# Performance work log

Hardware: AMD Instinct MI355X
Metric: run time of the kernel (lower is better)

The kernel has to match this reference:

```python
import jax, jax.numpy as jnp
import numpy as np

N, D_IN, D_H, D_ATT, C_CLUST, N_CLS = 10000, 1024, 512, 256, 10, 4


def setup_inputs() -> dict:
    key = jax.random.key(0)
    ks = jax.random.split(key, 20)
    s = 0.02
    return {
        "x": jax.random.normal(ks[0], (N, D_IN), dtype=jnp.float32),
        "cluster_id": jax.random.randint(ks[1], (N,), 0, C_CLUST, dtype=jnp.int64),
        # per-cluster phi: Linear(1024->512) + ReLU + Linear(512->512) + ReLU
        "W1": s * jax.random.normal(ks[2], (C_CLUST, D_IN, D_H), dtype=jnp.float32),
        "b1": jnp.zeros((C_CLUST, D_H), dtype=jnp.float32),
        "W2": s * jax.random.normal(ks[3], (C_CLUST, D_H, D_H), dtype=jnp.float32),
        "b2": jnp.zeros((C_CLUST, D_H), dtype=jnp.float32),
        # attention_net fc: Linear(512->512)+ReLU
        "Wfc": s * jax.random.normal(ks[4], (D_H, D_H), dtype=jnp.float32),
        "bfc": jnp.zeros((D_H,), dtype=jnp.float32),
        # Attn_Net_Gated
        "Wa": s * jax.random.normal(ks[5], (D_H, D_ATT), dtype=jnp.float32),
        "ba": jnp.zeros((D_ATT,), dtype=jnp.float32),
        "Wb": s * jax.random.normal(ks[6], (D_H, D_ATT), dtype=jnp.float32),
        "bb": jnp.zeros((D_ATT,), dtype=jnp.float32),
        "Wc": s * jax.random.normal(ks[7], (D_ATT, 1), dtype=jnp.float32),
        "bc": jnp.zeros((1,), dtype=jnp.float32),
        # rho: Linear(512->256)+ReLU
        "Wr": s * jax.random.normal(ks[8], (D_H, D_ATT), dtype=jnp.float32),
        "br": jnp.zeros((D_ATT,), dtype=jnp.float32),
        # classifier: Linear(256->4)
        "Wcls": s * jax.random.normal(ks[9], (D_ATT, N_CLS), dtype=jnp.float32),
        "bcls": jnp.zeros((N_CLS,), dtype=jnp.float32),
    }


def reference(x, cluster_id, W1, b1, W2, b2, Wfc, bfc, Wa, ba, Wb, bb, Wc, bc, Wr, br, Wcls, bcls):
    C = W1.shape[0]
    # dense dispatch: apply every cluster's phi, then masked-mean per cluster
    # (ReLU is per-point elementwise, so masked mean == mean over members)
    h1 = jax.nn.relu(jnp.einsum('nd,cdh->cnh', x, W1) + b1[:, None, :])   # [C,N,512]
    h2 = jax.nn.relu(jnp.einsum('cnh,chk->cnk', h1, W2) + b2[:, None, :]) # [C,N,512]
    mask = (cluster_id[None, :] == jnp.arange(C)[:, None]).astype(h2.dtype)  # [C,N]
    counts = jnp.maximum(mask.sum(axis=1), 1.0)                           # [C]
    pooled = jnp.einsum('cnk,cn->ck', h2, mask) / counts[:, None]         # [C,512]
    # attention_net: fc + gated attention
    h = jax.nn.relu(pooled @ Wfc + bfc)                                   # [C,512]
    gate = jnp.tanh(h @ Wa + ba) * jax.nn.sigmoid(h @ Wb + bb)            # [C,256]
    A = (gate @ Wc + bc)                                                  # [C,1]
    A = jax.nn.softmax(A.T, axis=1)                                       # [1,C]
    h_path = A @ h                                                        # [1,512]
    hr = jax.nn.relu(h_path @ Wr + br)                                    # [1,256]
    logits = (hr[0] @ Wcls + bcls)[None, :]                               # [1,4]
    Y_prob = jax.nn.softmax(logits, axis=1)
    Y_hat = jnp.argmax(logits, axis=1)[:, None]
    return logits, Y_prob, Y_hat
```

## Files before the change

kernel.cpp:

```cpp
#include <hip/hip_runtime.h>
#include <math.h>

#define DIN 1024
#define DH 512
#define DATT 256
#define CNUM 10
#define NCLS 4
#define NH 64
#define NSC 40

typedef __attribute__((ext_vector_type(8))) short bf16x8;
typedef __attribute__((ext_vector_type(4))) float f32x4;
typedef unsigned short ushort_t;
typedef unsigned int uint_t;

__device__ inline ushort_t f2bf(float f) {
    uint_t u = __float_as_uint(f);
    u += 0x7FFF + ((u >> 16) & 1);
    return (ushort_t)(u >> 16);
}

__device__ inline void gl_lds16(const void* g, void* l) {
    __builtin_amdgcn_global_load_lds(
        (const __attribute__((address_space(1))) unsigned int*)g,
        (__attribute__((address_space(3))) unsigned int*)l, 16, 0, 0);
}


__global__ __launch_bounds__(256) void k_hist(
    const int* __restrict__ cid, int n, const float* __restrict__ bc,
    int* __restrict__ counts_part, float* __restrict__ pooled,
    float* __restrict__ a_logit, int* __restrict__ scat_pos)
{
    int bid = blockIdx.x;
    int t = threadIdx.x;

    if (bid < NH) {
        __shared__ int h[CNUM];
        int lane = t & 63;
        if (t < CNUM) h[t] = 0;
        __syncthreads();
        for (int i = bid * 256 + t; i < n; i += NH * 256) {
            int c = cid[i];
            #pragma unroll
            for (int cc = 0; cc < CNUM; cc++) {
                unsigned long long mask = __ballot(c == cc);
                if (mask == 0ull) continue;
                if (lane == (__ffsll(mask) - 1)) atomicAdd(&h[cc], __popcll(mask));
            }
        }
        __syncthreads();
        if (t < CNUM) counts_part[bid * 16 + t] = h[t];
        return;
    }

    for (int i = t; i < CNUM * DH; i += 256) pooled[i] = 0.f;
    if (t < CNUM) a_logit[t] = bc[0];
    if (t < CNUM) scat_pos[t] = 0;
}


__global__ __launch_bounds__(256) void k_scat2(
    const int* __restrict__ cid, int n, const int* __restrict__ counts_part,
    const float* __restrict__ x, const float* __restrict__ W1, const float* __restrict__ W2,
    ushort_t* __restrict__ xb, ushort_t* __restrict__ W1t, ushort_t* __restrict__ W2t,
    int nxb, int nw,
    int* __restrict__ counts, int* __restrict__ offsets, int* __restrict__ tile_off,
    int* __restrict__ scat_pos, int* __restrict__ bucket)
{
    int bid = blockIdx.x;
    int t = threadIdx.x;

    if (bid < NSC) {
        __shared__ int cnts[CNUM], off[CNUM];
        if (t < CNUM) {
            int s = 0;
            #pragma unroll 8
            for (int b = 0; b < NH; b++) s += counts_part[b * 16 + t];
            cnts[t] = s;
        }
        __syncthreads();
        if (t == 0) {
            int a = 0;
            for (int c = 0; c < CNUM; c++) { off[c] = a; a += cnts[c]; }
            if (bid == 0) {
                int aa = 0, tt = 0;
                for (int c = 0; c < CNUM; c++) {
                    offsets[c] = aa; tile_off[c] = tt; counts[c] = cnts[c];
                    aa += cnts[c]; tt += (cnts[c] + 127) >> 7;
                }
                offsets[CNUM] = aa; tile_off[CNUM] = tt;
            }
        }
        __syncthreads();
        int lane = t & 63;
        for (int i = bid * 256 + t; i < n; i += NSC * 256) {
            int c = cid[i];
            #pragma unroll
            for (int cc = 0; cc < CNUM; cc++) {
                unsigned long long mask = __ballot(c == cc);
                if (mask == 0ull) continue;
                int leader = __ffsll(mask) - 1;
                int basep = 0;
                if (lane == leader) basep = atomicAdd(&scat_pos[cc], __popcll(mask));
                basep = __shfl(basep, leader, 64);
                if (c == cc) {
                    int rank = __popcll(mask & ((1ull << lane) - 1ull));
                    bucket[off[cc] + basep + rank] = i;
                }
            }
        }
        return;
    }
    bid -= NSC;

    if (bid < nxb) {
        int row = bid * 2 + (t >> 7);
        if (row >= n) return;
        int col = (t & 127) * 8;
        const float* src = x + (size_t)row * DIN + col;
        float4 v0 = *(const float4*)(src);
        float4 v1 = *(const float4*)(src + 4);
        ushort_t* dst = xb + (size_t)row * DIN + col;
        *(ushort4*)dst = make_ushort4(f2bf(v0.x), f2bf(v0.y), f2bf(v0.z), f2bf(v0.w));
        *(ushort4*)(dst + 4) = make_ushort4(f2bf(v1.x), f2bf(v1.y), f2bf(v1.z), f2bf(v1.w));
        return;
    }
    bid -= nxb;

    if (bid < nw) {
        __shared__ float tile[64][65];
        int z = bid >> 7;
        int kx = (bid & 127) >> 3;
        int ny = bid & 7;
        const float* src; ushort_t* dst; int K;
        if (z < CNUM) { K = DIN; src = W1 + (size_t)z * K * DH; dst = W1t + (size_t)z * DH * K; }
        else          { K = DH;  src = W2 + (size_t)(z - CNUM) * K * DH; dst = W2t + (size_t)(z - CNUM) * DH * K; }
        int k0 = kx * 64;
        if (k0 >= K) return;
        int n0 = ny * 64;
        int rr = t >> 4;
        int cc = (t & 15) * 4;
        #pragma unroll
        for (int i = 0; i < 4; i++) {
            int row = rr + 16 * i;
            float4 v = *(const float4*)(src + (size_t)(k0 + row) * DH + n0 + cc);
            tile[row][cc + 0] = v.x; tile[row][cc + 1] = v.y;
            tile[row][cc + 2] = v.z; tile[row][cc + 3] = v.w;
        }
        __syncthreads();
        #pragma unroll
        for (int i = 0; i < 4; i++) {
            int nrow = rr + 16 * i;
            ushort4 o = make_ushort4(f2bf(tile[cc + 0][nrow]), f2bf(tile[cc + 1][nrow]),
                                     f2bf(tile[cc + 2][nrow]), f2bf(tile[cc + 3][nrow]));
            *(ushort4*)(dst + (size_t)(n0 + nrow) * K + k0 + cc) = o;
        }
    }
}


__device__ inline void gemm_tile(
    const ushort_t* aSrc0, const ushort_t* aSrc1,
    const ushort_t* bSrc0, const ushort_t* bSrc1, int Kd,
    f32x4 acc[4][4], ushort_t As[128][32], ushort_t Bs[128][32])
{
    int t = threadIdx.x;
    int lane = t & 63;
    int w = t >> 6, wr = w >> 1, wc = w & 1;
    int m = lane & 15, quad = lane >> 4;

    int r0 = t >> 2;
    int kc = (t & 3) * 8;

    ushort_t* aDst0 = &As[r0][kc];
    ushort_t* aDst1 = &As[64 + r0][kc];
    ushort_t* bDst0 = &Bs[r0][kc];
    ushort_t* bDst1 = &Bs[64 + r0][kc];

    const ushort_t* aF = &As[64 * wr + m][quad * 8];
    const ushort_t* bF = &Bs[64 * wc + m][quad * 8];

    for (int k0 = 0; k0 < Kd; k0 += 32) {
        __syncthreads();
        gl_lds16(aSrc0 + k0, aDst0);
        gl_lds16(aSrc1 + k0, aDst1);
        gl_lds16(bSrc0 + k0, bDst0);
        gl_lds16(bSrc1 + k0, bDst1);
        __syncthreads();
        bf16x8 a[4], b[4];
        #pragma unroll
        for (int mf = 0; mf < 4; mf++) a[mf] = *(const bf16x8*)(aF + mf * 16 * 32);
        #pragma unroll
        for (int nf = 0; nf < 4; nf++) b[nf] = *(const bf16x8*)(bF + nf * 16 * 32);
        #pragma unroll
        for (int mf = 0; mf < 4; mf++)
            #pragma unroll
            for (int nf = 0; nf < 4; nf++)
                acc[mf][nf] = __builtin_amdgcn_mfma_f32_16x16x32_bf16(a[mf], b[nf], acc[mf][nf], 0, 0, 0);
    }
}

__global__ __launch_bounds__(256, 1) void k_mfma1(
    const ushort_t* __restrict__ xb, const ushort_t* __restrict__ W1t,
    const float* __restrict__ b1, const int* __restrict__ bucket,
    const int* __restrict__ offsets, const int* __restrict__ counts,
    const int* __restrict__ tile_off,
    ushort_t* __restrict__ H1)
{
    __shared__ ushort_t As[128][32];
    __shared__ ushort_t Bs[128][32];
    int tx = blockIdx.y;
    if (tx >= tile_off[CNUM]) return;
    int c = 0;
    while (tx >= tile_off[c + 1]) c++;
    int m0 = (tx - tile_off[c]) * 128;
    int base = offsets[c], cnt = counts[c];
    int tile_n = blockIdx.x * 128;

    int t = threadIdx.x;
    int r0 = t >> 2;
    int kc = (t & 3) * 8;
    int ra0 = m0 + r0;      if (ra0 > cnt - 1) ra0 = cnt - 1; if (ra0 < 0) ra0 = 0;
    int ra1 = m0 + 64 + r0; if (ra1 > cnt - 1) ra1 = cnt - 1; if (ra1 < 0) ra1 = 0;
    const ushort_t* aSrc0 = xb + (size_t)bucket[base + ra0] * DIN + kc;
    const ushort_t* aSrc1 = xb + (size_t)bucket[base + ra1] * DIN + kc;
    const ushort_t* bSrc0 = W1t + ((size_t)c * DH + tile_n + r0) * DIN + kc;
    const ushort_t* bSrc1 = W1t + ((size_t)c * DH + tile_n + 64 + r0) * DIN + kc;

    f32x4 acc[4][4] = {};
    gemm_tile(aSrc0, aSrc1, bSrc0, bSrc1, DIN, acc, As, Bs);

    int lane = t & 63;
    int w = t >> 6, wr = w >> 1, wc = w & 1;
    int m = lane & 15, quad = lane >> 4;
    int col0 = tile_n + 64 * wc;
    #pragma unroll
    for (int nf = 0; nf < 4; nf++) {
        int col = col0 + 16 * nf + m;
        float bv = b1[c * DH + col];
        #pragma unroll
        for (int mf = 0; mf < 4; mf++) {
            int rowb = m0 + 64 * wr + 16 * mf + quad * 4;
            #pragma unroll
            for (int r = 0; r < 4; r++) {
                int row = rowb + r;
                if (row < cnt)
                    H1[(size_t)(base + row) * DH + col] = f2bf(fmaxf(acc[mf][nf][r] + bv, 0.f));
            }
        }
    }
}

__global__ __launch_bounds__(256, 1) void k_mfma2(
    const ushort_t* __restrict__ H1, const ushort_t* __restrict__ W2t,
    const float* __restrict__ b2,
    const int* __restrict__ offsets, const int* __restrict__ counts,
    const int* __restrict__ tile_off,
    float* __restrict__ pooled)
{
    __shared__ ushort_t As[128][32];
    __shared__ ushort_t Bs[128][32];
    int tx = blockIdx.y;
    if (tx >= tile_off[CNUM]) return;
    int c = 0;
    while (tx >= tile_off[c + 1]) c++;
    int m0 = (tx - tile_off[c]) * 128;
    int base = offsets[c], cnt = counts[c];
    int tile_n = blockIdx.x * 128;

    int t = threadIdx.x;
    int r0 = t >> 2;
    int kc = (t & 3) * 8;
    int ra0 = m0 + r0;      if (ra0 > cnt - 1) ra0 = cnt - 1; if (ra0 < 0) ra0 = 0;
    int ra1 = m0 + 64 + r0; if (ra1 > cnt - 1) ra1 = cnt - 1; if (ra1 < 0) ra1 = 0;
    const ushort_t* aSrc0 = H1 + (size_t)(base + ra0) * DH + kc;
    const ushort_t* aSrc1 = H1 + (size_t)(base + ra1) * DH + kc;
    const ushort_t* bSrc0 = W2t + ((size_t)c * DH + tile_n + r0) * DH + kc;
    const ushort_t* bSrc1 = W2t + ((size_t)c * DH + tile_n + 64 + r0) * DH + kc;

    f32x4 acc[4][4] = {};
    gemm_tile(aSrc0, aSrc1, bSrc0, bSrc1, DH, acc, As, Bs);

    int lane = t & 63;
    int w = t >> 6, wr = w >> 1, wc = w & 1;
    int m = lane & 15, quad = lane >> 4;
    int col0 = tile_n + 64 * wc;
    #pragma unroll
    for (int nf = 0; nf < 4; nf++) {
        int col = col0 + 16 * nf + m;
        float bv = b2[c * DH + col];
        float s = 0.f;
        #pragma unroll
        for (int mf = 0; mf < 4; mf++) {
            int rowb = m0 + 64 * wr + 16 * mf + quad * 4;
            #pragma unroll
            for (int r = 0; r < 4; r++) {
                int row = rowb + r;
                if (row < cnt) s += fmaxf(acc[mf][nf][r] + bv, 0.f);
            }
        }
        s += __shfl_xor(s, 16);
        s += __shfl_xor(s, 32);
        if (quad == 0) atomicAdd(&pooled[c * DH + col], s);
    }
}


__global__ __launch_bounds__(256) void k_fc2(
    const float* __restrict__ pooled, const int* __restrict__ counts,
    const float* __restrict__ Wfc, const float* __restrict__ bfc,
    float* __restrict__ hfc)
{
    int c = blockIdx.x;
    int c0 = blockIdx.y * 64;
    __shared__ float ps[DH];
    __shared__ float red[4][64];
    int t = threadIdx.x;
    float cnt = fmaxf((float)counts[c], 1.f);
    ps[t] = pooled[c * DH + t] / cnt;
    ps[t + 256] = pooled[c * DH + t + 256] / cnt;
    __syncthreads();
    int col = c0 + (t & 63);
    int ks = t >> 6;
    float acc = 0.f;
    #pragma unroll 8
    for (int k = ks * 128; k < ks * 128 + 128; k++)
        acc = fmaf(ps[k], Wfc[(size_t)k * DH + col], acc);
    red[ks][t & 63] = acc;
    __syncthreads();
    if (t < 64) {
        float v = red[0][t] + red[1][t] + red[2][t] + red[3][t] + bfc[c0 + t];
        hfc[c * DH + c0 + t] = fmaxf(v, 0.f);
    }
}

__global__ __launch_bounds__(256) void k_gate2(
    const float* __restrict__ hfc,
    const float* __restrict__ Wa, const float* __restrict__ ba,
    const float* __restrict__ Wb, const float* __restrict__ bb,
    const float* __restrict__ Wc,
    float* __restrict__ a_logit)
{
    int c = blockIdx.x;
    int d0 = blockIdx.y * 64;
    __shared__ float hf[DH];
    __shared__ float ra[4][64], rb[4][64];
    int t = threadIdx.x;
    hf[t] = hfc[c * DH + t];
    hf[t + 256] = hfc[c * DH + t + 256];
    __syncthreads();
    int d = d0 + (t & 63);
    int ks = t >> 6;
    float ga = 0.f, gb = 0.f;
    #pragma unroll 8
    for (int k = ks * 128; k < ks * 128 + 128; k++) {
        float h = hf[k];
        ga = fmaf(h, Wa[(size_t)k * DATT + d], ga);
        gb = fmaf(h, Wb[(size_t)k * DATT + d], gb);
    }
    ra[ks][t & 63] = ga;
    rb[ks][t & 63] = gb;
    __syncthreads();
    if (t < 64) {
        float sa = ra[0][t] + ra[1][t] + ra[2][t] + ra[3][t] + ba[d0 + t];
        float sb = rb[0][t] + rb[1][t] + rb[2][t] + rb[3][t] + bb[d0 + t];
        float g = tanhf(sa) * (1.f / (1.f + expf(-sb)));
        float p = g * Wc[d0 + t];
        #pragma unroll
        for (int off = 32; off >= 1; off >>= 1) p += __shfl_down(p, off, 64);
        if (t == 0) atomicAdd(&a_logit[c], p);
    }
}

__global__ __launch_bounds__(1024) void k_final(
    const float* __restrict__ hfc, const float* __restrict__ a_logit,
    const float* __restrict__ Wr, const float* __restrict__ br,
    const float* __restrict__ Wcls, const float* __restrict__ bcls,
    float* __restrict__ out)
{
    int t = threadIdx.x;
    __shared__ float hp[DH];
    __shared__ float r1[4][DATT];
    __shared__ float hr[DATT];
    __shared__ float wred[4][NCLS];

    float al[CNUM];
    float m = -1e30f;
    #pragma unroll
    for (int c = 0; c < CNUM; c++) { al[c] = a_logit[c]; m = fmaxf(m, al[c]); }
    float s = 0.f;
    #pragma unroll
    for (int c = 0; c < CNUM; c++) { al[c] = expf(al[c] - m); s += al[c]; }
    float inv = 1.f / s;

    if (t < DH) {
        float v = 0.f;
        #pragma unroll
        for (int c = 0; c < CNUM; c++) v = fmaf(al[c] * inv, hfc[c * DH + t], v);
        hp[t] = v;
    }
    __syncthreads();

    int d = t & 255;
    int ks = t >> 8;
    float acc = 0.f;
    #pragma unroll 8
    for (int k = ks * 128; k < ks * 128 + 128; k++)
        acc = fmaf(hp[k], Wr[(size_t)k * DATT + d], acc);
    r1[ks][d] = acc;
    __syncthreads();
    if (t < DATT)
        hr[t] = fmaxf(r1[0][t] + r1[1][t] + r1[2][t] + r1[3][t] + br[t], 0.f);
    __syncthreads();

    if (t < 256) {
        float h = hr[t];
        #pragma unroll
        for (int cls = 0; cls < NCLS; cls++) {
            float p = h * Wcls[(size_t)t * NCLS + cls];
            #pragma unroll
            for (int off = 32; off >= 1; off >>= 1) p += __shfl_down(p, off, 64);
            if ((t & 63) == 0) wred[t >> 6][cls] = p;
        }
    }
    __syncthreads();
    if (t == 0) {
        float lg[NCLS];
        #pragma unroll
        for (int cls = 0; cls < NCLS; cls++)
            lg[cls] = bcls[cls] + wred[0][cls] + wred[1][cls] + wred[2][cls] + wred[3][cls];
        float mm = lg[0];
        #pragma unroll
        for (int i = 1; i < NCLS; i++) mm = fmaxf(mm, lg[i]);
        float ss = 0.f, pr[NCLS];
        #pragma unroll
        for (int i = 0; i < NCLS; i++) { pr[i] = expf(lg[i] - mm); ss += pr[i]; }
        int am = 0; float best = lg[0];
        #pragma unroll
        for (int i = 1; i < NCLS; i++) if (lg[i] > best) { best = lg[i]; am = i; }
        #pragma unroll
        for (int i = 0; i < NCLS; i++) out[i] = lg[i];
        #pragma unroll
        for (int i = 0; i < NCLS; i++) out[4 + i] = pr[i] / ss;
        out[8] = (float)am;
    }
}


#define MT 64
#define NT 128
#define KT 32

__global__ __launch_bounds__(256) void k_gemm1(
    const float* __restrict__ x, const float* __restrict__ W1, const float* __restrict__ b1,
    const int* __restrict__ bucket, const int* __restrict__ offsets, const int* __restrict__ counts,
    float* __restrict__ H1)
{
    int c = blockIdx.z;
    int cnt = counts[c];
    int m0 = blockIdx.x * MT;
    if (m0 >= cnt) return;
    int rows = min(MT, cnt - m0);
    int n0 = blockIdx.y * NT;
    int base = offsets[c];

    __shared__ float As[KT][MT + 4];
    __shared__ float Bs[KT][NT];

    int t = threadIdx.x;
    int tr = t >> 4;
    int tc = t & 15;
    int lr = t >> 2;
    int lk = (t & 3) * 8;
    const float* xrow = nullptr;
    if (lr < rows) xrow = x + (size_t)bucket[base + m0 + lr] * DIN;

    float acc[4][8];
    #pragma unroll
    for (int i = 0; i < 4; i++)
        #pragma unroll
        for (int j = 0; j < 8; j++) acc[i][j] = 0.f;

    const float* Wp = W1 + (size_t)c * DIN * DH + n0;

    for (int k0 = 0; k0 < DIN; k0 += KT) {
        __syncthreads();
        if (xrow) {
            float4 v0 = *(const float4*)(xrow + k0 + lk);
            float4 v1 = *(const float4*)(xrow + k0 + lk + 4);
            As[lk + 0][lr] = v0.x; As[lk + 1][lr] = v0.y;
            As[lk + 2][lr] = v0.z; As[lk + 3][lr] = v0.w;
            As[lk + 4][lr] = v1.x; As[lk + 5][lr] = v1.y;
            As[lk + 6][lr] = v1.z; As[lk + 7][lr] = v1.w;
        } else {
            #pragma unroll
            for (int i = 0; i < 8; i++) As[lk + i][lr] = 0.f;
        }
        #pragma unroll
        for (int i = 0; i < 4; i++) {
            int idx = i * 256 + t;
            int kk = idx >> 5;
            int cv = idx & 31;
            *(float4*)&Bs[kk][cv * 4] = *(const float4*)(Wp + (size_t)(k0 + kk) * DH + cv * 4);
        }
        __syncthreads();
        #pragma unroll
        for (int k = 0; k < KT; k++) {
            float4 av  = *(const float4*)&As[k][4 * tr];
            float4 bv0 = *(const float4*)&Bs[k][4 * tc];
            float4 bv1 = *(const float4*)&Bs[k][64 + 4 * tc];
            float a[4] = {av.x, av.y, av.z, av.w};
            float b[8] = {bv0.x, bv0.y, bv0.z, bv0.w, bv1.x, bv1.y, bv1.z, bv1.w};
            #pragma unroll
            for (int i = 0; i < 4; i++)
                #pragma unroll
                for (int j = 0; j < 8; j++)
                    acc[i][j] = fmaf(a[i], b[j], acc[i][j]);
        }
    }

    #pragma unroll
    for (int i = 0; i < 4; i++) {
        int r = 4 * tr + i;
        if (r < rows) {
            size_t grow = (size_t)(base + m0 + r) * DH;
            #pragma unroll
            for (int j = 0; j < 8; j++) {
                int cidx = (j < 4) ? (4 * tc + j) : (64 + 4 * tc + (j - 4));
                int col = n0 + cidx;
                float v = acc[i][j] + b1[c * DH + col];
                H1[grow + col] = fmaxf(v, 0.f);
            }
        }
    }
}

__global__ __launch_bounds__(256) void k_gemm2(
    const float* __restrict__ H1, const float* __restrict__ W2, const float* __restrict__ b2,
    const int* __restrict__ offsets, const int* __restrict__ counts,
    float* __restrict__ pooled)
{
    int c = blockIdx.z;
    int cnt = counts[c];
    int m0 = blockIdx.x * MT;
    if (m0 >= cnt) return;
    int rows = min(MT, cnt - m0);
    int n0 = blockIdx.y * NT;
    int base = offsets[c];

    __shared__ float As[KT][MT + 4];
    __shared__ float Bs[KT][NT];
    __shared__ float red[16][NT];

    int t = threadIdx.x;
    int tr = t >> 4;
    int tc = t & 15;
    int lr = t >> 2;
    int lk = (t & 3) * 8;
    const float* arow = (lr < rows) ? (H1 + (size_t)(base + m0 + lr) * DH) : nullptr;

    float acc[4][8];
    #pragma unroll
    for (int i = 0; i < 4; i++)
        #pragma unroll
        for (int j = 0; j < 8; j++) acc[i][j] = 0.f;

    const float* Wp = W2 + (size_t)c * DH * DH + n0;

    for (int k0 = 0; k0 < DH; k0 += KT) {
        __syncthreads();
        if (arow) {
            float4 v0 = *(const float4*)(arow + k0 + lk);
            float4 v1 = *(const float4*)(arow + k0 + lk + 4);
            As[lk + 0][lr] = v0.x; As[lk + 1][lr] = v0.y;
            As[lk + 2][lr] = v0.z; As[lk + 3][lr] = v0.w;
            As[lk + 4][lr] = v1.x; As[lk + 5][lr] = v1.y;
            As[lk + 6][lr] = v1.z; As[lk + 7][lr] = v1.w;
        } else {
            #pragma unroll
            for (int i = 0; i < 8; i++) As[lk + i][lr] = 0.f;
        }
        #pragma unroll
        for (int i = 0; i < 4; i++) {
            int idx = i * 256 + t;
            int kk = idx >> 5;
            int cv = idx & 31;
            *(float4*)&Bs[kk][cv * 4] = *(const float4*)(Wp + (size_t)(k0 + kk) * DH + cv * 4);
        }
        __syncthreads();
        #pragma unroll
        for (int k = 0; k < KT; k++) {
            float4 av  = *(const float4*)&As[k][4 * tr];
            float4 bv0 = *(const float4*)&Bs[k][4 * tc];
            float4 bv1 = *(const float4*)&Bs[k][64 + 4 * tc];
            float a[4] = {av.x, av.y, av.z, av.w};
            float b[8] = {bv0.x, bv0.y, bv0.z, bv0.w, bv1.x, bv1.y, bv1.z, bv1.w};
            #pragma unroll
            for (int i = 0; i < 4; i++)
                #pragma unroll
                for (int j = 0; j < 8; j++)
                    acc[i][j] = fmaf(a[i], b[j], acc[i][j]);
        }
    }

    __syncthreads();
    #pragma unroll
    for (int j = 0; j < 8; j++) {
        int cidx = (j < 4) ? (4 * tc + j) : (64 + 4 * tc + (j - 4));
        float bias = b2[c * DH + n0 + cidx];
        float s = 0.f;
        #pragma unroll
        for (int i = 0; i < 4; i++) {
            if (4 * tr + i < rows) s += fmaxf(acc[i][j] + bias, 0.f);
        }
        red[tr][cidx] = s;
    }
    __syncthreads();
    if (t < NT) {
        float s = 0.f;
        #pragma unroll
        for (int r = 0; r < 16; r++) s += red[r][t];
        atomicAdd(&pooled[c * DH + n0 + t], s);
    }
}


extern "C" void kernel_launch(void* const* d_in, const int* in_sizes, int n_in,
                              void* d_out, int out_size, void* d_ws, size_t ws_size,
                              hipStream_t stream) {
    (void)n_in; (void)out_size;
    const float* x    = (const float*)d_in[0];
    const int*   cid  = (const int*)d_in[1];
    const float* W1   = (const float*)d_in[2];
    const float* b1   = (const float*)d_in[3];
    const float* W2   = (const float*)d_in[4];
    const float* b2   = (const float*)d_in[5];
    const float* Wfc  = (const float*)d_in[6];
    const float* bfc  = (const float*)d_in[7];
    const float* Wa   = (const float*)d_in[8];
    const float* ba   = (const float*)d_in[9];
    const float* Wb   = (const float*)d_in[10];
    const float* bb   = (const float*)d_in[11];
    const float* Wc   = (const float*)d_in[12];
    const float* bc   = (const float*)d_in[13];
    const float* Wr   = (const float*)d_in[14];
    const float* br   = (const float*)d_in[15];
    const float* Wcls = (const float*)d_in[16];
    const float* bcls = (const float*)d_in[17];
    float* out = (float*)d_out;
    float* ws  = (float*)d_ws;

    int n = in_sizes[1];

    float* pooled     = ws + 0;
    int*   counts     = (int*)(ws + 5120);
    int*   offsets    = (int*)(ws + 5136);
    int*   tile_off   = (int*)(ws + 5152);
    float* a_logit    = ws + 5168;
    int*   scat_pos   = (int*)(ws + 5184);
    float* hfc        = ws + 5200;
    int*   counts_part= (int*)(ws + 10320);
    int*   bucket     = (int*)(ws + 11344);

    size_t big0 = (((size_t)(11344 + n) * 4) + 255) & ~(size_t)255;
    size_t w1t_bytes = (size_t)CNUM * DH * DIN * 2;
    size_t w2t_bytes = (size_t)CNUM * DH * DH * 2;
    size_t h1_bytes  = (size_t)n * DH * 2;
    size_t xb_bytes  = (size_t)n * DIN * 2;
    size_t need = big0 + w1t_bytes + w2t_bytes + h1_bytes + xb_bytes;

    ushort_t* W1t = (ushort_t*)((char*)d_ws + big0);
    ushort_t* W2t = (ushort_t*)((char*)d_ws + big0 + w1t_bytes);
    ushort_t* H1  = (ushort_t*)((char*)d_ws + big0 + w1t_bytes + w2t_bytes);
    ushort_t* xb  = (ushort_t*)((char*)d_ws + big0 + w1t_bytes + w2t_bytes + h1_bytes);

    int fast = (ws_size >= need) ? 1 : 0;
    int nxb = fast ? (n + 1) / 2 : 0;
    int nw  = fast ? 128 * 2 * CNUM : 0;

    k_hist<<<NH + 1, 256, 0, stream>>>(cid, n, bc, counts_part, pooled, a_logit, scat_pos);
    k_scat2<<<NSC + nxb + nw, 256, 0, stream>>>(
        cid, n, counts_part, x, W1, W2, xb, W1t, W2t, nxb, nw,
        counts, offsets, tile_off, scat_pos, bucket);

    if (fast) {
        int maxt = n / 128 + CNUM;
        k_mfma1<<<dim3(4, maxt), 256, 0, stream>>>(xb, W1t, b1, bucket, offsets, counts, tile_off, H1);
        k_mfma2<<<dim3(4, maxt), 256, 0, stream>>>(H1, W2t, b2, offsets, counts, tile_off, pooled);
    } else {
        float* H1f = ws + ((11344 + n + 31) & ~31);
        dim3 gg((n + MT - 1) / MT, DH / NT, CNUM);
        k_gemm1<<<gg, 256, 0, stream>>>(x, W1, b1, bucket, offsets, counts, H1f);
        k_gemm2<<<gg, 256, 0, stream>>>(H1f, W2, b2, offsets, counts, pooled);
    }

    k_fc2<<<dim3(CNUM, 8), 256, 0, stream>>>(pooled, counts, Wfc, bfc, hfc);
    k_gate2<<<dim3(CNUM, 4), 256, 0, stream>>>(hfc, Wa, ba, Wb, bb, Wc, a_logit);
    k_final<<<1, 1024, 0, stream>>>(hfc, a_logit, Wr, br, Wcls, bcls, out);
}
```

Baseline: 231.3 us.

## Reshape grouped GEMM tiles to 256x64 and reduce pooled partials in LDS

The per-cluster MFMA GEMMs change from 128x128 tiles to 256-row by 64-column tiles. Each wave now owns 64 rows and the full 64 columns, and tile bookkeeping is recomputed in 256-row units. The second GEMM adds its four wave partial sums through shared memory before a single atomic per column, which cuts global atomics fourfold. The new shape loads more gathered A data per k-step and less B data, and creates fewer padded tiles per cluster, at the cost of a different load balance across blocks and a larger LDS A buffer.

```diff
diff --git a/kernel.cpp b/kernel.cpp
--- a/kernel.cpp
+++ b/kernel.cpp
@@ -87,7 +87,7 @@
                 int aa = 0, tt = 0;
                 for (int c = 0; c < CNUM; c++) {
                     offsets[c] = aa; tile_off[c] = tt; counts[c] = cnts[c];
-                    aa += cnts[c]; tt += (cnts[c] + 127) >> 7;
+                    aa += cnts[c]; tt += (cnts[c] + 255) >> 8;
                 }
                 offsets[CNUM] = aa; tile_off[CNUM] = tt;
             }
@@ -160,14 +160,15 @@
 }
 
 
-__device__ inline void gemm_tile(
+__device__ inline void gemm_tile256(
     const ushort_t* aSrc0, const ushort_t* aSrc1,
-    const ushort_t* bSrc0, const ushort_t* bSrc1, int Kd,
-    f32x4 acc[4][4], ushort_t As[128][32], ushort_t Bs[128][32])
+    const ushort_t* aSrc2, const ushort_t* aSrc3,
+    const ushort_t* bSrc, int Kd,
+    f32x4 acc[4][4], ushort_t As[256][32], ushort_t Bs[64][32])
 {
     int t = threadIdx.x;
     int lane = t & 63;
-    int w = t >> 6, wr = w >> 1, wc = w & 1;
+    int w = t >> 6;
     int m = lane & 15, quad = lane >> 4;
 
     int r0 = t >> 2;
@@ -175,18 +176,20 @@
 
     ushort_t* aDst0 = &As[r0][kc];
     ushort_t* aDst1 = &As[64 + r0][kc];
-    ushort_t* bDst0 = &Bs[r0][kc];
-    ushort_t* bDst1 = &Bs[64 + r0][kc];
-
-    const ushort_t* aF = &As[64 * wr + m][quad * 8];
-    const ushort_t* bF = &Bs[64 * wc + m][quad * 8];
+    ushort_t* aDst2 = &As[128 + r0][kc];
+    ushort_t* aDst3 = &As[192 + r0][kc];
+    ushort_t* bDst  = &Bs[r0][kc];
+
+    const ushort_t* aF = &As[64 * w + m][quad * 8];
+    const ushort_t* bF = &Bs[m][quad * 8];
 
     for (int k0 = 0; k0 < Kd; k0 += 32) {
         __syncthreads();
         gl_lds16(aSrc0 + k0, aDst0);
         gl_lds16(aSrc1 + k0, aDst1);
-        gl_lds16(bSrc0 + k0, bDst0);
-        gl_lds16(bSrc1 + k0, bDst1);
+        gl_lds16(aSrc2 + k0, aDst2);
+        gl_lds16(aSrc3 + k0, aDst3);
+        gl_lds16(bSrc + k0, bDst);
         __syncthreads();
         bf16x8 a[4], b[4];
         #pragma unroll
@@ -208,40 +211,41 @@
     const int* __restrict__ tile_off,
     ushort_t* __restrict__ H1)
 {
-    __shared__ ushort_t As[128][32];
-    __shared__ ushort_t Bs[128][32];
+    __shared__ ushort_t As[256][32];
+    __shared__ ushort_t Bs[64][32];
     int tx = blockIdx.y;
     if (tx >= tile_off[CNUM]) return;
     int c = 0;
     while (tx >= tile_off[c + 1]) c++;
-    int m0 = (tx - tile_off[c]) * 128;
+    int m0 = (tx - tile_off[c]) * 256;
     int base = offsets[c], cnt = counts[c];
-    int tile_n = blockIdx.x * 128;
+    int tile_n = blockIdx.x * 64;
 
     int t = threadIdx.x;
     int r0 = t >> 2;
     int kc = (t & 3) * 8;
-    int ra0 = m0 + r0;      if (ra0 > cnt - 1) ra0 = cnt - 1; if (ra0 < 0) ra0 = 0;
-    int ra1 = m0 + 64 + r0; if (ra1 > cnt - 1) ra1 = cnt - 1; if (ra1 < 0) ra1 = 0;
-    const ushort_t* aSrc0 = xb + (size_t)bucket[base + ra0] * DIN + kc;
-    const ushort_t* aSrc1 = xb + (size_t)bucket[base + ra1] * DIN + kc;
-    const ushort_t* bSrc0 = W1t + ((size_t)c * DH + tile_n + r0) * DIN + kc;
-    const ushort_t* bSrc1 = W1t + ((size_t)c * DH + tile_n + 64 + r0) * DIN + kc;
+    const ushort_t* aS[4];
+    #pragma unroll
+    for (int i = 0; i < 4; i++) {
+        int ra = m0 + 64 * i + r0;
+        if (ra > cnt - 1) ra = cnt - 1;
+        aS[i] = xb + (size_t)bucket[base + ra] * DIN + kc;
+    }
+    const ushort_t* bSrc = W1t + ((size_t)c * DH + tile_n + r0) * DIN + kc;
 
     f32x4 acc[4][4] = {};
-    gemm_tile(aSrc0, aSrc1, bSrc0, bSrc1, DIN, acc, As, Bs);
+    gemm_tile256(aS[0], aS[1], aS[2], aS[3], bSrc, DIN, acc, As, Bs);
 
     int lane = t & 63;
-    int w = t >> 6, wr = w >> 1, wc = w & 1;
+    int w = t >> 6;
     int m = lane & 15, quad = lane >> 4;
-    int col0 = tile_n + 64 * wc;
     #pragma unroll
     for (int nf = 0; nf < 4; nf++) {
-        int col = col0 + 16 * nf + m;
+        int col = tile_n + 16 * nf + m;
         float bv = b1[c * DH + col];
         #pragma unroll
         for (int mf = 0; mf < 4; mf++) {
-            int rowb = m0 + 64 * wr + 16 * mf + quad * 4;
+            int rowb = m0 + 64 * w + 16 * mf + quad * 4;
             #pragma unroll
             for (int r = 0; r < 4; r++) {
                 int row = rowb + r;
@@ -259,41 +263,43 @@
     const int* __restrict__ tile_off,
     float* __restrict__ pooled)
 {
-    __shared__ ushort_t As[128][32];
-    __shared__ ushort_t Bs[128][32];
+    __shared__ ushort_t As[256][32];
+    __shared__ ushort_t Bs[64][32];
+    __shared__ float red2[4][64];
     int tx = blockIdx.y;
     if (tx >= tile_off[CNUM]) return;
     int c = 0;
     while (tx >= tile_off[c + 1]) c++;
-    int m0 = (tx - tile_off[c]) * 128;
+    int m0 = (tx - tile_off[c]) * 256;
     int base = offsets[c], cnt = counts[c];
-    int tile_n = blockIdx.x * 128;
+    int tile_n = blockIdx.x * 64;
 
     int t = threadIdx.x;
     int r0 = t >> 2;
     int kc = (t & 3) * 8;
-    int ra0 = m0 + r0;      if (ra0 > cnt - 1) ra0 = cnt - 1; if (ra0 < 0) ra0 = 0;
-    int ra1 = m0 + 64 + r0; if (ra1 > cnt - 1) ra1 = cnt - 1; if (ra1 < 0) ra1 = 0;
-    const ushort_t* aSrc0 = H1 + (size_t)(base + ra0) * DH + kc;
-    const ushort_t* aSrc1 = H1 + (size_t)(base + ra1) * DH + kc;
-    const ushort_t* bSrc0 = W2t + ((size_t)c * DH + tile_n + r0) * DH + kc;
-    const ushort_t* bSrc1 = W2t + ((size_t)c * DH + tile_n + 64 + r0) * DH + kc;
+    const ushort_t* aS[4];
+    #pragma unroll
+    for (int i = 0; i < 4; i++) {
+        int ra = m0 + 64 * i + r0;
+        if (ra > cnt - 1) ra = cnt - 1;
+        aS[i] = H1 + (size_t)(base + ra) * DH + kc;
+    }
+    const ushort_t* bSrc = W2t + ((size_t)c * DH + tile_n + r0) * DH + kc;
 
     f32x4 acc[4][4] = {};
-    gemm_tile(aSrc0, aSrc1, bSrc0, bSrc1, DH, acc, As, Bs);
+    gemm_tile256(aS[0], aS[1], aS[2], aS[3], bSrc, DH, acc, As, Bs);
 
     int lane = t & 63;
-    int w = t >> 6, wr = w >> 1, wc = w & 1;
+    int w = t >> 6;
     int m = lane & 15, quad = lane >> 4;
-    int col0 = tile_n + 64 * wc;
     #pragma unroll
     for (int nf = 0; nf < 4; nf++) {
-        int col = col0 + 16 * nf + m;
+        int col = tile_n + 16 * nf + m;
         float bv = b2[c * DH + col];
         float s = 0.f;
         #pragma unroll
         for (int mf = 0; mf < 4; mf++) {
-            int rowb = m0 + 64 * wr + 16 * mf + quad * 4;
+            int rowb = m0 + 64 * w + 16 * mf + quad * 4;
             #pragma unroll
             for (int r = 0; r < 4; r++) {
                 int row = rowb + r;
@@ -302,7 +308,12 @@
         }
         s += __shfl_xor(s, 16);
         s += __shfl_xor(s, 32);
-        if (quad == 0) atomicAdd(&pooled[c * DH + col], s);
+        if (quad == 0) red2[w][16 * nf + m] = s;
+    }
+    __syncthreads();
+    if (t < 64) {
+        float s = red2[0][t] + red2[1][t] + red2[2][t] + red2[3][t];
+        atomicAdd(&pooled[c * DH + tile_n + t], s);
     }
 }
 
@@ -685,9 +696,9 @@
         counts, offsets, tile_off, scat_pos, bucket);
 
     if (fast) {
-        int maxt = n / 128 + CNUM;
-        k_mfma1<<<dim3(4, maxt), 256, 0, stream>>>(xb, W1t, b1, bucket, offsets, counts, tile_off, H1);
-        k_mfma2<<<dim3(4, maxt), 256, 0, stream>>>(H1, W2t, b2, offsets, counts, tile_off, pooled);
+        int maxt = n / 256 + CNUM;
+        k_mfma1<<<dim3(8, maxt), 256, 0, stream>>>(xb, W1t, b1, bucket, offsets, counts, tile_off, H1);
+        k_mfma2<<<dim3(8, maxt), 256, 0, stream>>>(H1, W2t, b2, offsets, counts, tile_off, pooled);
     } else {
         float* H1f = ws + ((11344 + n + 31) & ~31);
         dim3 gg((n + MT - 1) / MT, DH / NT, CNUM);
```

After: 241.4 us. +4.4%, slower.
